# Performance work log

Hardware: AMD Instinct MI355X
Metric: run time of the kernel (lower is better)

Reference implementation:

```python
import jax, jax.numpy as jnp
import numpy as np
import math

B, N, HID, NH = 128, 512, 512, 8
DH = HID // NH  # d_heads = 64


def setup_inputs() -> dict:
    key = jax.random.key(0)
    ks = jax.random.split(key, 8)
    s = 0.05  # keep logits in a sane range
    h = jax.random.normal(ks[0], (B, N, HID), dtype=jnp.float32)
    lengths = jax.random.randint(ks[1], (B,), 1, N + 1, dtype=jnp.int32)
    w_q = jax.random.normal(ks[2], (HID, HID), dtype=jnp.float32) * s
    w_k = jax.random.normal(ks[3], (HID, HID), dtype=jnp.float32) * s
    w_v = jax.random.normal(ks[4], (HID, HID), dtype=jnp.float32) * s
    w_o = jax.random.normal(ks[5], (HID, HID), dtype=jnp.float32) * s
    w_seed_w = jax.random.normal(ks[6], (HID, 1), dtype=jnp.float32) * s  # Linear(1, k*hidden), k=1
    w_seed_b = jax.random.normal(ks[7], (HID,), dtype=jnp.float32) * s
    seed_vec = jnp.ones((1,), dtype=jnp.float32)
    return {"h": h, "lengths": lengths, "w_q": w_q, "w_k": w_k, "w_v": w_v,
            "w_o": w_o, "w_seed_w": w_seed_w, "w_seed_b": w_seed_b, "seed_vec": seed_vec}


def reference(h, lengths, w_q, w_k, w_v, w_o, w_seed_w, w_seed_b, seed_vec):
    # PMA with k=1 seed query. norm_features=False.
    # query = w_seed(seed_vec), same for every graph in the batch.
    query = w_seed_w @ seed_vec + w_seed_b            # [HID]
    q = (w_q @ query).reshape(NH, DH)                 # [NH, DH] (Linear: x @ W.T == W @ x for vector)
    # NOTE: original code computes w_k(v) but never uses it in attention; output
    # depends only on q and v (e = q * v summed over d_heads). We skip the dead compute.
    v = (h @ w_v.T).reshape(B, N, NH, DH)             # [B, N, NH, DH]
    # logits: e[b,h,n] = <q[h], v[b,n,h]> / sqrt(DH)
    e = jnp.einsum("hd,bnhd->bhn", q, v) / math.sqrt(DH)
    valid = jnp.arange(N)[None, :] < lengths[:, None]  # [B, N] ragged mask
    e = jnp.where(valid[:, None, :], e, -jnp.inf)
    alpha = jax.nn.softmax(e, axis=-1)                # [B, NH, N]; padded cols -> 0
    out_h = jnp.einsum("bhn,bnhd->bhd", alpha, v)     # [B, NH, DH]
    out = out_h.reshape(B, HID) @ w_o.T               # [B*k, HID], packed (k=1)
    alpha_out = alpha[..., None]                      # [B, NH, N, 1] matching torch permute
    return out, alpha_out
```

## Files before the change

kernel.cpp:

```cpp
#include <hip/hip_runtime.h>
#include <math.h>

constexpr int B = 128, N = 512, HID = 512, NH = 8, DH = 64;

__global__ __launch_bounds__(64) void k1_qk(
    const float* __restrict__ w_q, const float* __restrict__ w_v,
    const float* __restrict__ w_sw, const float* __restrict__ w_sb,
    const float* __restrict__ seed, float* __restrict__ qk)
{
    __shared__ __align__(16) float query_s[HID];
    __shared__ float q_s[DH];
    const int t  = threadIdx.x;
    const int h  = blockIdx.x >> 3;
    const int jc = blockIdx.x & 7;
    const float sv = seed[0];
    #pragma unroll
    for (int k = 0; k < 8; ++k) {
        const int j = t * 8 + k;
        query_s[j] = w_sw[j] * sv + w_sb[j];
    }
    __syncthreads();
    {
        const float* row = w_q + (size_t)(h * DH + t) * HID;
        float acc = 0.f;
        for (int j = 0; j < HID; j += 4) {
            const float4 wv = *(const float4*)(row + j);
            acc += wv.x * query_s[j]     + wv.y * query_s[j + 1]
                 + wv.z * query_s[j + 2] + wv.w * query_s[j + 3];
        }
        q_s[t] = acc;
    }
    __syncthreads();
    {
        const int j = jc * 64 + t;
        float acc = 0.f;
        for (int d = 0; d < DH; ++d)
            acc += q_s[d] * w_v[(size_t)(h * DH + d) * HID + j];
        qk[h * HID + j] = acc * 0.125f;
    }
}

__global__ __launch_bounds__(256) void k2_e(
    const float* __restrict__ hbuf, const int* __restrict__ lengths,
    const float* __restrict__ qk, float* __restrict__ e_ws)
{
    __shared__ float part[2][2][64][9];
    const int t    = threadIdx.x;
    const int lane = t & 63;
    const int wave = t >> 6;
    const int b    = blockIdx.x >> 2;
    const int c    = blockIdx.x & 3;
    const int g    = __builtin_amdgcn_readfirstlane(wave >> 1);
    const int hb   = __builtin_amdgcn_readfirstlane(wave & 1);
    const int n    = c * 128 + g * 64 + lane;
    const int len  = lengths[b];

    float acc[NH];
    #pragma unroll
    for (int hh = 0; hh < NH; ++hh) acc[hh] = 0.f;

    if (n < len) {
        const float* row = hbuf + (size_t)(b * N + n) * HID + hb * 256;
        const float* qkb = qk + hb * 256;
        #pragma unroll 4
        for (int q = 0; q < 256; q += 8) {
            const float4 h0 = *(const float4*)(row + q);
            const float4 h1 = *(const float4*)(row + q + 4);
            #pragma unroll
            for (int hh = 0; hh < NH; ++hh) {
                const float* qp = qkb + hh * HID + q;
                acc[hh] += h0.x * qp[0] + h0.y * qp[1] + h0.z * qp[2] + h0.w * qp[3]
                         + h1.x * qp[4] + h1.y * qp[5] + h1.z * qp[6] + h1.w * qp[7];
            }
        }
    }
    #pragma unroll
    for (int hh = 0; hh < NH; ++hh)
        part[g][hb][lane][hh] = acc[hh];
    __syncthreads();

    #pragma unroll
    for (int v = t; v < 2 * 64 * NH; v += 256) {
        const int gg = v >> 9, r = (v >> 3) & 63, hh = v & 7;
        const int n2 = c * 128 + gg * 64 + r;
        if (n2 < len)
            e_ws[(size_t)(b * NH + hh) * N + n2] =
                part[gg][0][r][hh] + part[gg][1][r][hh];
    }
}

__global__ __launch_bounds__(256) void k2b_softmax(
    const float* __restrict__ e_ws, const int* __restrict__ lengths,
    float* __restrict__ alpha, float* __restrict__ al_t)
{
    const int b    = blockIdx.x;
    const int lane = threadIdx.x & 63;
    const int w    = threadIdx.x >> 6;
    const int len  = lengths[b];
    for (int hh = w; hh < NH; hh += 4) {
        const float* e = e_ws + (size_t)(b * NH + hh) * N;
        float ev[8];
        float m = -3.0e38f;
        #pragma unroll
        for (int it = 0; it < 8; ++it) {
            const int n = it * 64 + lane;
            ev[it] = (n < len) ? e[n] : -3.0e38f;
            m = fmaxf(m, ev[it]);
        }
        #pragma unroll
        for (int off = 32; off; off >>= 1)
            m = fmaxf(m, __shfl_xor(m, off, 64));
        float s = 0.f;
        #pragma unroll
        for (int it = 0; it < 8; ++it) {
            ev[it] = __expf(ev[it] - m);
            s += ev[it];
        }
        #pragma unroll
        for (int off = 32; off; off >>= 1)
            s += __shfl_xor(s, off, 64);
        const float inv = 1.f / s;
        float* ao = alpha + (size_t)(b * NH + hh) * N;
        float* at = al_t + (size_t)b * N * NH + hh;
        #pragma unroll
        for (int it = 0; it < 8; ++it) {
            const int n   = it * 64 + lane;
            const float v = (n < len) ? ev[it] * inv : 0.f;
            ao[n]         = v;
            at[n * NH]    = v;
        }
    }
}

__global__ __launch_bounds__(256) void k3_ctx(
    const float* __restrict__ hbuf, const int* __restrict__ lengths,
    const float* __restrict__ al_t, float* __restrict__ ctxp)
{
    const int t   = threadIdx.x;
    const int b   = blockIdx.x >> 3;
    const int c   = blockIdx.x & 7;
    const int n0  = c * 64;
    const int len = lengths[b];
    const int nend = min(len - n0, 64);

    float2 acc[NH];
    #pragma unroll
    for (int hh = 0; hh < NH; ++hh) { acc[hh].x = 0.f; acc[hh].y = 0.f; }

    const float* hb = hbuf + (size_t)(b * N + n0) * HID + t * 2;
    const float* ap = al_t + (size_t)(b * N + n0) * NH;
    #pragma unroll 2
    for (int ln = 0; ln < nend; ++ln) {
        const float2 hv = *(const float2*)(hb + (size_t)ln * HID);
        const float* a = ap + ln * NH;
        acc[0].x += a[0] * hv.x; acc[0].y += a[0] * hv.y;
        acc[1].x += a[1] * hv.x; acc[1].y += a[1] * hv.y;
        acc[2].x += a[2] * hv.x; acc[2].y += a[2] * hv.y;
        acc[3].x += a[3] * hv.x; acc[3].y += a[3] * hv.y;
        acc[4].x += a[4] * hv.x; acc[4].y += a[4] * hv.y;
        acc[5].x += a[5] * hv.x; acc[5].y += a[5] * hv.y;
        acc[6].x += a[6] * hv.x; acc[6].y += a[6] * hv.y;
        acc[7].x += a[7] * hv.x; acc[7].y += a[7] * hv.y;
    }
    #pragma unroll
    for (int hh = 0; hh < NH; ++hh)
        *(float2*)&ctxp[(size_t)((b * 8 + c) * NH + hh) * HID + t * 2] = acc[hh];
}

__global__ __launch_bounds__(256) void k4_out(
    const float* __restrict__ ctxp, const float* __restrict__ w_v,
    const float* __restrict__ w_o, float* __restrict__ out)
{
    __shared__ __align__(16) float ctx_s[NH * HID];
    __shared__ __align__(16) float oh_s[HID];
    const int t = threadIdx.x;
    const int b = blockIdx.x;
    const float* p0 = ctxp + (size_t)(b * 8) * NH * HID;
    for (int i = t; i < NH * HID; i += 256) {
        float s = 0.f;
        #pragma unroll
        for (int cc = 0; cc < 8; ++cc) s += p0[cc * NH * HID + i];
        ctx_s[i] = s;
    }
    __syncthreads();
    #pragma unroll
    for (int rep = 0; rep < 2; ++rep) {
        const int p  = rep * 256 + t;
        const int hh = p >> 6;
        const float* wrow = w_v + (size_t)p * HID;
        float acc = 0.f;
        for (int j = 0; j < HID; j += 4) {
            const float4 wv = *(const float4*)(wrow + j);
            const float4 cv = *(const float4*)&ctx_s[hh * HID + j];
            acc += wv.x * cv.x + wv.y * cv.y + wv.z * cv.z + wv.w * cv.w;
        }
        oh_s[p] = acc;
    }
    __syncthreads();
    #pragma unroll
    for (int rep = 0; rep < 2; ++rep) {
        const int i = rep * 256 + t;
        const float* wrow = w_o + (size_t)i * HID;
        float acc = 0.f;
        for (int j = 0; j < HID; j += 4) {
            const float4 wv = *(const float4*)(wrow + j);
            const float4 ov = *(const float4*)&oh_s[j];
            acc += wv.x * ov.x + wv.y * ov.y + wv.z * ov.z + wv.w * ov.w;
        }
        out[(size_t)b * HID + i] = acc;
    }
}

extern "C" void kernel_launch(void* const* d_in, const int* in_sizes, int n_in,
                              void* d_out, int out_size, void* d_ws, size_t ws_size,
                              hipStream_t stream) {
    const float* h     = (const float*)d_in[0];
    const int*   lens  = (const int*)  d_in[1];
    const float* w_q   = (const float*)d_in[2];
    const float* w_v   = (const float*)d_in[4];
    const float* w_o   = (const float*)d_in[5];
    const float* w_sw  = (const float*)d_in[6];
    const float* w_sb  = (const float*)d_in[7];
    const float* seed  = (const float*)d_in[8];

    float* out   = (float*)d_out;
    float* alpha = out + (size_t)B * HID;

    float* ws   = (float*)d_ws;
    float* qk   = ws;
    float* e_ws = qk + NH * HID;
    float* al_t = e_ws + (size_t)B * NH * N;
    float* ctxp = al_t + (size_t)B * N * NH;

    hipLaunchKernelGGL(k1_qk,       dim3(64),    dim3(64),  0, stream,
                       w_q, w_v, w_sw, w_sb, seed, qk);
    hipLaunchKernelGGL(k2_e,        dim3(B * 4), dim3(256), 0, stream,
                       h, lens, qk, e_ws);
    hipLaunchKernelGGL(k2b_softmax, dim3(B),     dim3(256), 0, stream,
                       e_ws, lens, alpha, al_t);
    hipLaunchKernelGGL(k3_ctx,      dim3(B * 8), dim3(256), 0, stream,
                       h, lens, al_t, ctxp);
    hipLaunchKernelGGL(k4_out,      dim3(B),     dim3(256), 0, stream,
                       ctxp, w_v, w_o, out);
}
```

Before: 305.7 us.

## Restructure logits and context kernels: one row per thread, float4 ctx with split rows

The logits kernel now assigns one full token row per thread and writes results directly, which removes the shared-memory partial reduction and the barrier. Waves whose tokens all lie past the sequence length exit early, and tail threads clamp their row index. The context kernel moves to float4 loads, with two thread groups each taking alternate rows, so the number of partial buffers doubles to 16 per batch and the output kernel sums 16 partials. In exchange, each logits thread reads its own full 2KB row uncoalesced across lanes, and the final reduction handles more partial traffic.

```diff
diff --git a/kernel.cpp b/kernel.cpp
--- a/kernel.cpp
+++ b/kernel.cpp
@@ -40,56 +40,42 @@
     }
 }
 
-__global__ __launch_bounds__(256) void k2_e(
+__global__ __launch_bounds__(256) void ke_logits(
     const float* __restrict__ hbuf, const int* __restrict__ lengths,
     const float* __restrict__ qk, float* __restrict__ e_ws)
 {
-    __shared__ float part[2][2][64][9];
     const int t    = threadIdx.x;
-    const int lane = t & 63;
-    const int wave = t >> 6;
-    const int b    = blockIdx.x >> 2;
-    const int c    = blockIdx.x & 3;
-    const int g    = __builtin_amdgcn_readfirstlane(wave >> 1);
-    const int hb   = __builtin_amdgcn_readfirstlane(wave & 1);
-    const int n    = c * 128 + g * 64 + lane;
+    const int b    = blockIdx.x >> 1;
+    const int half = blockIdx.x & 1;
     const int len  = lengths[b];
-
+    const int n    = half * 256 + t;
+    const int n0   = half * 256 + (t & ~63);
+    if (n0 >= len) return;
+
+    const int nn = min(n, len - 1);
+    const float* row = hbuf + ((size_t)b * N + nn) * HID;
     float acc[NH];
     #pragma unroll
     for (int hh = 0; hh < NH; ++hh) acc[hh] = 0.f;
 
+    #pragma unroll 8
+    for (int j = 0; j < HID; j += 4) {
+        const float4 hv = *(const float4*)(row + j);
+        #pragma unroll
+        for (int hh = 0; hh < NH; ++hh) {
+            const float* qp = qk + hh * HID + j;
+            acc[hh] += hv.x * qp[0] + hv.y * qp[1]
+                     + hv.z * qp[2] + hv.w * qp[3];
+        }
+    }
     if (n < len) {
-        const float* row = hbuf + (size_t)(b * N + n) * HID + hb * 256;
-        const float* qkb = qk + hb * 256;
-        #pragma unroll 4
-        for (int q = 0; q < 256; q += 8) {
-            const float4 h0 = *(const float4*)(row + q);
-            const float4 h1 = *(const float4*)(row + q + 4);
-            #pragma unroll
-            for (int hh = 0; hh < NH; ++hh) {
-                const float* qp = qkb + hh * HID + q;
-                acc[hh] += h0.x * qp[0] + h0.y * qp[1] + h0.z * qp[2] + h0.w * qp[3]
-                         + h1.x * qp[4] + h1.y * qp[5] + h1.z * qp[6] + h1.w * qp[7];
-            }
-        }
-    }
-    #pragma unroll
-    for (int hh = 0; hh < NH; ++hh)
-        part[g][hb][lane][hh] = acc[hh];
-    __syncthreads();
-
-    #pragma unroll
-    for (int v = t; v < 2 * 64 * NH; v += 256) {
-        const int gg = v >> 9, r = (v >> 3) & 63, hh = v & 7;
-        const int n2 = c * 128 + gg * 64 + r;
-        if (n2 < len)
-            e_ws[(size_t)(b * NH + hh) * N + n2] =
-                part[gg][0][r][hh] + part[gg][1][r][hh];
-    }
-}
-
-__global__ __launch_bounds__(256) void k2b_softmax(
+        #pragma unroll
+        for (int hh = 0; hh < NH; ++hh)
+            e_ws[(size_t)(b * NH + hh) * N + n] = acc[hh];
+    }
+}
+
+__global__ __launch_bounds__(256) void ks_softmax(
     const float* __restrict__ e_ws, const int* __restrict__ lengths,
     float* __restrict__ alpha, float* __restrict__ al_t)
 {
@@ -126,13 +112,13 @@
         for (int it = 0; it < 8; ++it) {
             const int n   = it * 64 + lane;
             const float v = (n < len) ? ev[it] * inv : 0.f;
-            ao[n]         = v;
-            at[n * NH]    = v;
-        }
-    }
-}
-
-__global__ __launch_bounds__(256) void k3_ctx(
+            ao[n]      = v;
+            at[n * NH] = v;
+        }
+    }
+}
+
+__global__ __launch_bounds__(256) void kc_ctx(
     const float* __restrict__ hbuf, const int* __restrict__ lengths,
     const float* __restrict__ al_t, float* __restrict__ ctxp)
 {
@@ -140,34 +126,37 @@
     const int b   = blockIdx.x >> 3;
     const int c   = blockIdx.x & 7;
     const int n0  = c * 64;
+    const int g   = t >> 7;
+    const int cq  = t & 127;
     const int len = lengths[b];
     const int nend = min(len - n0, 64);
 
-    float2 acc[NH];
-    #pragma unroll
-    for (int hh = 0; hh < NH; ++hh) { acc[hh].x = 0.f; acc[hh].y = 0.f; }
-
-    const float* hb = hbuf + (size_t)(b * N + n0) * HID + t * 2;
-    const float* ap = al_t + (size_t)(b * N + n0) * NH;
-    #pragma unroll 2
-    for (int ln = 0; ln < nend; ++ln) {
-        const float2 hv = *(const float2*)(hb + (size_t)ln * HID);
+    float4 acc[NH];
+    #pragma unroll
+    for (int hh = 0; hh < NH; ++hh) { acc[hh].x = acc[hh].y = acc[hh].z = acc[hh].w = 0.f; }
+
+    const float* hb = hbuf + ((size_t)b * N + n0) * HID + cq * 4;
+    const float* ap = al_t + ((size_t)b * N + n0) * NH;
+    #pragma unroll 4
+    for (int ln = g; ln < nend; ln += 2) {
+        const float4 hv = *(const float4*)(hb + (size_t)ln * HID);
         const float* a = ap + ln * NH;
-        acc[0].x += a[0] * hv.x; acc[0].y += a[0] * hv.y;
-        acc[1].x += a[1] * hv.x; acc[1].y += a[1] * hv.y;
-        acc[2].x += a[2] * hv.x; acc[2].y += a[2] * hv.y;
-        acc[3].x += a[3] * hv.x; acc[3].y += a[3] * hv.y;
-        acc[4].x += a[4] * hv.x; acc[4].y += a[4] * hv.y;
-        acc[5].x += a[5] * hv.x; acc[5].y += a[5] * hv.y;
-        acc[6].x += a[6] * hv.x; acc[6].y += a[6] * hv.y;
-        acc[7].x += a[7] * hv.x; acc[7].y += a[7] * hv.y;
-    }
+        acc[0].x += a[0] * hv.x; acc[0].y += a[0] * hv.y; acc[0].z += a[0] * hv.z; acc[0].w += a[0] * hv.w;
+        acc[1].x += a[1] * hv.x; acc[1].y += a[1] * hv.y; acc[1].z += a[1] * hv.z; acc[1].w += a[1] * hv.w;
+        acc[2].x += a[2] * hv.x; acc[2].y += a[2] * hv.y; acc[2].z += a[2] * hv.z; acc[2].w += a[2] * hv.w;
+        acc[3].x += a[3] * hv.x; acc[3].y += a[3] * hv.y; acc[3].z += a[3] * hv.z; acc[3].w += a[3] * hv.w;
+        acc[4].x += a[4] * hv.x; acc[4].y += a[4] * hv.y; acc[4].z += a[4] * hv.z; acc[4].w += a[4] * hv.w;
+        acc[5].x += a[5] * hv.x; acc[5].y += a[5] * hv.y; acc[5].z += a[5] * hv.z; acc[5].w += a[5] * hv.w;
+        acc[6].x += a[6] * hv.x; acc[6].y += a[6] * hv.y; acc[6].z += a[6] * hv.z; acc[6].w += a[6] * hv.w;
+        acc[7].x += a[7] * hv.x; acc[7].y += a[7] * hv.y; acc[7].z += a[7] * hv.z; acc[7].w += a[7] * hv.w;
+    }
+    float* cp = ctxp + (size_t)(((b * 8 + c) * 2 + g) * NH) * HID + cq * 4;
     #pragma unroll
     for (int hh = 0; hh < NH; ++hh)
-        *(float2*)&ctxp[(size_t)((b * 8 + c) * NH + hh) * HID + t * 2] = acc[hh];
-}
-
-__global__ __launch_bounds__(256) void k4_out(
+        *(float4*)(cp + (size_t)hh * HID) = acc[hh];
+}
+
+__global__ __launch_bounds__(256) void kd_out(
     const float* __restrict__ ctxp, const float* __restrict__ w_v,
     const float* __restrict__ w_o, float* __restrict__ out)
 {
@@ -175,11 +164,11 @@
     __shared__ __align__(16) float oh_s[HID];
     const int t = threadIdx.x;
     const int b = blockIdx.x;
-    const float* p0 = ctxp + (size_t)(b * 8) * NH * HID;
+    const float* p0 = ctxp + (size_t)(b * 16) * NH * HID;
     for (int i = t; i < NH * HID; i += 256) {
         float s = 0.f;
         #pragma unroll
-        for (int cc = 0; cc < 8; ++cc) s += p0[cc * NH * HID + i];
+        for (int cc = 0; cc < 16; ++cc) s += p0[(size_t)cc * NH * HID + i];
         ctx_s[i] = s;
     }
     __syncthreads();
@@ -232,14 +221,14 @@
     float* al_t = e_ws + (size_t)B * NH * N;
     float* ctxp = al_t + (size_t)B * N * NH;
 
-    hipLaunchKernelGGL(k1_qk,       dim3(64),    dim3(64),  0, stream,
+    hipLaunchKernelGGL(k1_qk,      dim3(64),    dim3(64),  0, stream,
                        w_q, w_v, w_sw, w_sb, seed, qk);
-    hipLaunchKernelGGL(k2_e,        dim3(B * 4), dim3(256), 0, stream,
+    hipLaunchKernelGGL(ke_logits,  dim3(B * 2), dim3(256), 0, stream,
                        h, lens, qk, e_ws);
-    hipLaunchKernelGGL(k2b_softmax, dim3(B),     dim3(256), 0, stream,
+    hipLaunchKernelGGL(ks_softmax, dim3(B),     dim3(256), 0, stream,
                        e_ws, lens, alpha, al_t);
-    hipLaunchKernelGGL(k3_ctx,      dim3(B * 8), dim3(256), 0, stream,
+    hipLaunchKernelGGL(kc_ctx,     dim3(B * 8), dim3(256), 0, stream,
                        h, lens, al_t, ctxp);
-    hipLaunchKernelGGL(k4_out,      dim3(B),     dim3(256), 0, stream,
+    hipLaunchKernelGGL(kd_out,     dim3(B),     dim3(256), 0, stream,
                        ctxp, w_v, w_o, out);
 }
```

Result: slower. 331.6 us (+8.5%).
